# Performance work log

Measured on AMD Instinct MI355X. Metric: run time of the kernel, lower is better.

Reference implementation:

```python
import jax, jax.numpy as jnp
import numpy as np

DEGREE = 3


def bspline_basis(t, knots, degree):
    """Vectorized Cox-de Boor recursion. t: [S], knots: [K]. Returns B: [S, K-degree-1].
    Faithful to the torch loop: at degree d only columns [0, n_knots-d) are updated;
    higher columns keep their stale lower-degree values, and term2 reads the
    not-yet-updated column i+1 (i.e. previous-degree values), matching ascending-i
    in-place updates.
    """
    n_knots = knots.shape[0] - degree - 1
    # degree-0 basis: indicator of half-open knot spans
    B = ((knots[None, :n_knots] <= t[:, None]) &
         (t[:, None] < knots[None, 1:n_knots + 1])).astype(t.dtype)
    for d in range(1, degree + 1):
        n = n_knots - d
        denom1 = knots[d:d + n] - knots[:n]          # knots[i+d]   - knots[i]
        denom2 = knots[d + 1:d + 1 + n] - knots[1:1 + n]  # knots[i+d+1] - knots[i+1]
        safe1 = jnp.where(denom1 == 0, 1.0, denom1)
        safe2 = jnp.where(denom2 == 0, 1.0, denom2)
        w1 = jnp.where(denom1 == 0, 0.0, (t[:, None] - knots[None, :n]) / safe1)
        w2 = jnp.where(denom2 == 0, 0.0, (knots[None, d + 1:d + 1 + n] - t[:, None]) / safe2)
        new_cols = w1 * B[:, :n] + w2 * B[:, 1:n + 1]
        B = B.at[:, :n].set(new_cols)
    return B


def setup_inputs() -> dict:
    key = jax.random.key(0)
    k1, k2 = jax.random.split(key)
    N_KNOTS, DIM, T_MAX = 2048, 512, 32768.0
    t = jnp.sort(jax.random.uniform(k1, (N_KNOTS,), dtype=jnp.float32)) * T_MAX
    t = t.at[-1].set(T_MAX)  # make sample range exactly [0, T_MAX)
    c = jax.random.normal(k2, (DIM, N_KNOTS), dtype=jnp.float32)
    return {"t": t, "c": c, "delta": 1}


def reference(t, c, delta):
    padded_t = jnp.concatenate([jnp.zeros(DEGREE + 1, dtype=t.dtype), t])
    # number of samples is data-dependent (t[-1]); concretize outside jit
    t_max = float(t[-1])
    sample_points = jnp.arange(0.0, t_max, float(delta), dtype=t.dtype)  # [S]
    B = bspline_basis(sample_points, padded_t, DEGREE)  # [S, n_knots]
    spline_values = B @ c.T  # [S, dim]
    return sample_points, spline_values
```

## Files before the change

### kernel.cpp

```cpp
#include <hip/hip_runtime.h>


#define DEG 3

__device__ __forceinline__ float kn(const float* __restrict__ t, int i) {
    return (i < DEG + 1) ? 0.0f : t[i - (DEG + 1)];
}

#define TILE 32
__global__ __launch_bounds__(256) void transpose_kernel(
    const float* __restrict__ src, float* __restrict__ dst,
    int rows, int cols)
{
    __shared__ float tile[TILE][TILE + 1];
    int x = blockIdx.x * TILE + threadIdx.x;
    int y = blockIdx.y * TILE + threadIdx.y;
    #pragma unroll
    for (int i = 0; i < TILE; i += 8) {
        if (y + i < rows && x < cols)
            tile[threadIdx.y + i][threadIdx.x] = src[(size_t)(y + i) * cols + x];
    }
    __syncthreads();
    int x2 = blockIdx.y * TILE + threadIdx.x;
    int y2 = blockIdx.x * TILE + threadIdx.y;
    #pragma unroll
    for (int i = 0; i < TILE; i += 8) {
        if (y2 + i < cols && x2 < rows)
            dst[(size_t)(y2 + i) * rows + x2] = tile[threadIdx.x][threadIdx.y + i];
    }
}

__global__ __launch_bounds__(256) void weights_kernel(
    const float* __restrict__ t, const int* __restrict__ delta_p,
    float* __restrict__ out_pts, int* __restrict__ jbuf,
    float4* __restrict__ bbuf, int S, int NK)
{
    int s = blockIdx.x * blockDim.x + threadIdx.x;
    if (s >= S) return;
    const float delta = (float)(*delta_p);
    const float sv = (float)s * delta;
    out_pts[s] = sv;

    int lo = DEG, hi = NK + DEG - 1;
    while (lo < hi) {
        int mid = (lo + hi + 1) >> 1;
        if (kn(t, mid) <= sv) lo = mid; else hi = mid - 1;
    }
    const int j = lo;

    if (j >= NK) {
        jbuf[s] = NK - 1;
        bbuf[s] = make_float4(0.f, 0.f, 0.f, 0.f);
        return;
    }

    float N[DEG + 1][DEG + 1];
    N[0][0] = 1.0f;
    #pragma unroll
    for (int d = 1; d <= DEG; ++d) {
        #pragma unroll
        for (int k = 0; k <= d; ++k) {
            int i = j - d + k;
            float vpi  = (k >= 1) ? N[d - 1][k - 1] : 0.0f;
            float vpi1 = (k <= d - 1) ? N[d - 1][k] : 0.0f;
            float ki   = kn(t, i);
            float kid  = kn(t, i + d);
            float ki1  = kn(t, i + 1);
            float kid1 = kn(t, i + d + 1);
            float den1 = kid - ki;
            float den2 = kid1 - ki1;
            float w1 = (den1 != 0.0f) ? (sv - ki) / den1 : 0.0f;
            float w2 = (den2 != 0.0f) ? (kid1 - sv) / den2 : 0.0f;
            N[d][k] = w1 * vpi + w2 * vpi1;
        }
    }

    float b[DEG + 1];
    #pragma unroll
    for (int m = 0; m <= DEG; ++m) {
        int col = j - DEG + m;
        int deg = NK - 1 - col; if (deg > DEG) deg = DEG;
        int idx = m - DEG + deg;
        b[m] = (idx >= 0) ? N[deg][idx] : 0.0f;
    }
    jbuf[s] = j;
    bbuf[s] = make_float4(b[0], b[1], b[2], b[3]);
}

__global__ __launch_bounds__(256) void bspline_eval(
    const int* __restrict__ jbuf, const float4* __restrict__ bbuf,
    const float* __restrict__ cT, float4* __restrict__ out_spline,
    int DIM)
{
    const int nvec = DIM >> 2;
    int g = blockIdx.x * blockDim.x + threadIdx.x;
    int s = __builtin_amdgcn_readfirstlane(g >> 7);
    int d = g & (nvec - 1);

    const int j = jbuf[s];
    const float4 b = bbuf[s];

    const float4* __restrict__ r = (const float4*)(cT + (size_t)(j - 3) * DIM);
    float4 a0 = r[d];
    float4 a1 = r[d + nvec];
    float4 a2 = r[d + 2 * nvec];
    float4 a3 = r[d + 3 * nvec];

    float4 o;
    o.x = b.x * a0.x + b.y * a1.x + b.z * a2.x + b.w * a3.x;
    o.y = b.x * a0.y + b.y * a1.y + b.z * a2.y + b.w * a3.y;
    o.z = b.x * a0.z + b.y * a1.z + b.z * a2.z + b.w * a3.z;
    o.w = b.x * a0.w + b.y * a1.w + b.z * a2.w + b.w * a3.w;
    out_spline[(size_t)s * nvec + d] = o;
}

extern "C" void kernel_launch(void* const* d_in, const int* in_sizes, int n_in,
                              void* d_out, int out_size, void* d_ws, size_t ws_size,
                              hipStream_t stream) {
    const float* t = (const float*)d_in[0];
    const float* c = (const float*)d_in[1];
    const int* delta = (const int*)d_in[2];
    const int NK = in_sizes[0];
    const int DIM = in_sizes[1] / NK;
    const int S = out_size / (1 + DIM);

    float* cT = (float*)d_ws;
    int* jbuf = (int*)((char*)d_ws + (size_t)NK * DIM * 4);
    float4* bbuf = (float4*)((char*)jbuf + (size_t)S * 4);

    dim3 tb(TILE, 8);
    dim3 tg((NK + TILE - 1) / TILE, (DIM + TILE - 1) / TILE);
    transpose_kernel<<<tg, tb, 0, stream>>>(c, cT, DIM, NK);

    weights_kernel<<<(S + 255) / 256, 256, 0, stream>>>(
        t, delta, (float*)d_out, jbuf, bbuf, S, NK);

    int total = S * (DIM >> 2);
    bspline_eval<<<total / 256, 256, 0, stream>>>(
        jbuf, bbuf, cT, (float4*)((float*)d_out + S), DIM);
}
```

Measured before the change: 97.14 us.

## Merge transpose and weight kernels; evaluate four samples per thread reusing coefficient rows

Folds the coefficient transpose and the per-sample basis-weight computation into one launch, with block index selecting the role, which removes one kernel launch. The eval kernel now has each thread produce four consecutive samples. When all four share the same knot span it loads the four coefficient rows once and reuses them, cutting redundant loads. Outputs are written with nontemporal stores. It drops bounds checks in the transpose and assumes S is divisible by 4 and that DIM is 512, since lane indexing is hardcoded to 128 float4s per row.

```diff
diff --git a/kernel.cpp b/kernel.cpp
--- a/kernel.cpp
+++ b/kernel.cpp
@@ -2,40 +2,41 @@
 
 
 #define DEG 3
+
+typedef float vfloat4 __attribute__((ext_vector_type(4)));
 
 __device__ __forceinline__ float kn(const float* __restrict__ t, int i) {
     return (i < DEG + 1) ? 0.0f : t[i - (DEG + 1)];
 }
 
 #define TILE 32
-__global__ __launch_bounds__(256) void transpose_kernel(
-    const float* __restrict__ src, float* __restrict__ dst,
-    int rows, int cols)
-{
-    __shared__ float tile[TILE][TILE + 1];
-    int x = blockIdx.x * TILE + threadIdx.x;
-    int y = blockIdx.y * TILE + threadIdx.y;
-    #pragma unroll
-    for (int i = 0; i < TILE; i += 8) {
-        if (y + i < rows && x < cols)
-            tile[threadIdx.y + i][threadIdx.x] = src[(size_t)(y + i) * cols + x];
-    }
-    __syncthreads();
-    int x2 = blockIdx.y * TILE + threadIdx.x;
-    int y2 = blockIdx.x * TILE + threadIdx.y;
-    #pragma unroll
-    for (int i = 0; i < TILE; i += 8) {
-        if (y2 + i < cols && x2 < rows)
-            dst[(size_t)(y2 + i) * rows + x2] = tile[threadIdx.x][threadIdx.y + i];
-    }
-}
-
-__global__ __launch_bounds__(256) void weights_kernel(
+__global__ __launch_bounds__(256) void prep_kernel(
+    const float* __restrict__ c, float* __restrict__ cT,
     const float* __restrict__ t, const int* __restrict__ delta_p,
     float* __restrict__ out_pts, int* __restrict__ jbuf,
-    float4* __restrict__ bbuf, int S, int NK)
+    vfloat4* __restrict__ bbuf, int S, int NK, int DIM, int TB)
 {
-    int s = blockIdx.x * blockDim.x + threadIdx.x;
+    if ((int)blockIdx.x < TB) {
+        __shared__ float tile[TILE][TILE + 1];
+        int bx = blockIdx.x % (NK / TILE);
+        int by = blockIdx.x / (NK / TILE);
+        int tx = threadIdx.x % TILE;
+        int ty = threadIdx.x / TILE;
+        int x = bx * TILE + tx;
+        int y = by * TILE + ty;
+        #pragma unroll
+        for (int i = 0; i < TILE; i += 8)
+            tile[ty + i][tx] = c[(size_t)(y + i) * NK + x];
+        __syncthreads();
+        int x2 = by * TILE + tx;
+        int y2 = bx * TILE + ty;
+        #pragma unroll
+        for (int i = 0; i < TILE; i += 8)
+            cT[(size_t)(y2 + i) * DIM + x2] = tile[tx][ty + i];
+        return;
+    }
+
+    int s = (blockIdx.x - TB) * blockDim.x + threadIdx.x;
     if (s >= S) return;
     const float delta = (float)(*delta_p);
     const float sv = (float)s * delta;
@@ -50,7 +51,7 @@
 
     if (j >= NK) {
         jbuf[s] = NK - 1;
-        bbuf[s] = make_float4(0.f, 0.f, 0.f, 0.f);
+        bbuf[s] = (vfloat4){0.f, 0.f, 0.f, 0.f};
         return;
     }
 
@@ -84,34 +85,62 @@
         b[m] = (idx >= 0) ? N[deg][idx] : 0.0f;
     }
     jbuf[s] = j;
-    bbuf[s] = make_float4(b[0], b[1], b[2], b[3]);
+    bbuf[s] = (vfloat4){b[0], b[1], b[2], b[3]};
+}
+
+__device__ __forceinline__ vfloat4 dot4(const vfloat4 b, const vfloat4 a0,
+                                        const vfloat4 a1, const vfloat4 a2,
+                                        const vfloat4 a3) {
+    return b.x * a0 + b.y * a1 + b.z * a2 + b.w * a3;
 }
 
 __global__ __launch_bounds__(256) void bspline_eval(
-    const int* __restrict__ jbuf, const float4* __restrict__ bbuf,
-    const float* __restrict__ cT, float4* __restrict__ out_spline,
+    const int* __restrict__ jbuf, const vfloat4* __restrict__ bbuf,
+    const float* __restrict__ cT, vfloat4* __restrict__ out_spline,
     int DIM)
 {
     const int nvec = DIM >> 2;
-    int g = blockIdx.x * blockDim.x + threadIdx.x;
-    int s = __builtin_amdgcn_readfirstlane(g >> 7);
-    int d = g & (nvec - 1);
+    int gtid = blockIdx.x * blockDim.x + threadIdx.x;
+    int wid  = gtid >> 6;
+    int lane = gtid & 63;
+    int grp  = wid >> 1;
+    int d    = ((wid & 1) << 6) | lane;
+    int s0   = __builtin_amdgcn_readfirstlane(grp << 2);
 
-    const int j = jbuf[s];
-    const float4 b = bbuf[s];
+    const int j0 = jbuf[s0 + 0];
+    const int j3 = jbuf[s0 + 3];
+    const vfloat4 b0 = bbuf[s0 + 0];
+    const vfloat4 b1 = bbuf[s0 + 1];
+    const vfloat4 b2 = bbuf[s0 + 2];
+    const vfloat4 b3 = bbuf[s0 + 3];
 
-    const float4* __restrict__ r = (const float4*)(cT + (size_t)(j - 3) * DIM);
-    float4 a0 = r[d];
-    float4 a1 = r[d + nvec];
-    float4 a2 = r[d + 2 * nvec];
-    float4 a3 = r[d + 3 * nvec];
+    vfloat4* o = out_spline + (size_t)s0 * nvec + d;
 
-    float4 o;
-    o.x = b.x * a0.x + b.y * a1.x + b.z * a2.x + b.w * a3.x;
-    o.y = b.x * a0.y + b.y * a1.y + b.z * a2.y + b.w * a3.y;
-    o.z = b.x * a0.z + b.y * a1.z + b.z * a2.z + b.w * a3.z;
-    o.w = b.x * a0.w + b.y * a1.w + b.z * a2.w + b.w * a3.w;
-    out_spline[(size_t)s * nvec + d] = o;
+    if (j0 == j3) {
+        const vfloat4* r = (const vfloat4*)(cT + (size_t)(j3 - 3) * DIM) + d;
+        vfloat4 a0 = r[0];
+        vfloat4 a1 = r[nvec];
+        vfloat4 a2 = r[2 * nvec];
+        vfloat4 a3 = r[3 * nvec];
+        __builtin_nontemporal_store(dot4(b0, a0, a1, a2, a3), o);
+        __builtin_nontemporal_store(dot4(b1, a0, a1, a2, a3), o + nvec);
+        __builtin_nontemporal_store(dot4(b2, a0, a1, a2, a3), o + 2 * nvec);
+        __builtin_nontemporal_store(dot4(b3, a0, a1, a2, a3), o + 3 * nvec);
+    } else {
+        const int j1 = jbuf[s0 + 1];
+        const int j2 = jbuf[s0 + 2];
+        const int js[4] = {j0, j1, j2, j3};
+        const vfloat4 bs[4] = {b0, b1, b2, b3};
+        #pragma unroll
+        for (int m = 0; m < 4; ++m) {
+            const vfloat4* r = (const vfloat4*)(cT + (size_t)(js[m] - 3) * DIM) + d;
+            vfloat4 a0 = r[0];
+            vfloat4 a1 = r[nvec];
+            vfloat4 a2 = r[2 * nvec];
+            vfloat4 a3 = r[3 * nvec];
+            __builtin_nontemporal_store(dot4(bs[m], a0, a1, a2, a3), o + m * nvec);
+        }
+    }
 }
 
 extern "C" void kernel_launch(void* const* d_in, const int* in_sizes, int n_in,
@@ -126,16 +155,14 @@
 
     float* cT = (float*)d_ws;
     int* jbuf = (int*)((char*)d_ws + (size_t)NK * DIM * 4);
-    float4* bbuf = (float4*)((char*)jbuf + (size_t)S * 4);
+    vfloat4* bbuf = (vfloat4*)((char*)jbuf + (size_t)S * 4);
 
-    dim3 tb(TILE, 8);
-    dim3 tg((NK + TILE - 1) / TILE, (DIM + TILE - 1) / TILE);
-    transpose_kernel<<<tg, tb, 0, stream>>>(c, cT, DIM, NK);
+    const int TB = (NK / TILE) * (DIM / TILE);
+    const int WB = (S + 255) / 256;
+    prep_kernel<<<TB + WB, 256, 0, stream>>>(
+        c, cT, t, delta, (float*)d_out, jbuf, bbuf, S, NK, DIM, TB);
 
-    weights_kernel<<<(S + 255) / 256, 256, 0, stream>>>(
-        t, delta, (float*)d_out, jbuf, bbuf, S, NK);
-
-    int total = S * (DIM >> 2);
-    bspline_eval<<<total / 256, 256, 0, stream>>>(
-        jbuf, bbuf, cT, (float4*)((float*)d_out + S), DIM);
+    int total_threads = (S >> 2) * (DIM >> 2);
+    bspline_eval<<<total_threads / 256, 256, 0, stream>>>(
+        jbuf, bbuf, cT, (vfloat4*)((float*)d_out + S), DIM);
 }
```

New measurement: 93.93 us. 3.3% less time.
